# Performance work log

Measured on AMD Instinct MI355X. Metric: run time of the kernel, lower is better.

The kernel has to match this reference:

```python
import jax, jax.numpy as jnp
import numpy as np

EMBED = 2048
HEADS = 16
DFF = 4 * EMBED
EPS = 1e-5


def layernorm(x, g, b):
    mu = jnp.mean(x, axis=-1, keepdims=True)
    var = jnp.var(x, axis=-1, keepdims=True)
    return (x - mu) * jax.lax.rsqrt(var + EPS) * g + b


def setup_inputs() -> dict:
    key = jax.random.key(0)
    ks = jax.random.split(key, 16)
    s = 1.0 / np.sqrt(EMBED)
    sf = 1.0 / np.sqrt(DFF)
    return {
        "x": jax.random.normal(ks[0], (2, 2048, EMBED), jnp.float32),
        "Wq": jax.random.normal(ks[1], (EMBED, EMBED), jnp.float32) * s,
        "bq": jnp.zeros((EMBED,), jnp.float32),
        "Wk": jax.random.normal(ks[2], (EMBED, EMBED), jnp.float32) * s,
        "bk": jnp.zeros((EMBED,), jnp.float32),
        "Wv": jax.random.normal(ks[3], (EMBED, EMBED), jnp.float32) * s,
        "bv": jnp.zeros((EMBED,), jnp.float32),
        "Wo": jax.random.normal(ks[4], (EMBED, EMBED), jnp.float32) * s,
        "bo": jnp.zeros((EMBED,), jnp.float32),
        "g1": jnp.ones((EMBED,), jnp.float32),
        "b1": jnp.zeros((EMBED,), jnp.float32),
        "g2": jnp.ones((EMBED,), jnp.float32),
        "b2": jnp.zeros((EMBED,), jnp.float32),
        "W1": jax.random.normal(ks[5], (EMBED, DFF), jnp.float32) * s,
        "bf1": jnp.zeros((DFF,), jnp.float32),
        "W2": jax.random.normal(ks[6], (DFF, EMBED), jnp.float32) * sf,
        "bf2": jnp.zeros((EMBED,), jnp.float32),
    }


def reference(x, Wq, bq, Wk, bk, Wv, bv, Wo, bo, g1, b1, g2, b2, W1, bf1, W2, bf2):
    B, N, C = x.shape
    H = HEADS
    hd = C // H
    # QKV projections -> [B, H, N, hd]
    def split_heads(t):
        return t.reshape(B, N, H, hd).transpose(0, 2, 1, 3)
    q = split_heads(x @ Wq + bq)
    k = split_heads(x @ Wk + bk)
    v = split_heads(x @ Wv + bv)
    # scores [B, H, N, N]
    attn = jnp.einsum('bhqd,bhkd->bhqk', q, k) / np.sqrt(hd)
    attn = jax.nn.softmax(attn, axis=-1)
    out = jnp.einsum('bhqk,bhkd->bhqd', attn, v)
    out = out.transpose(0, 2, 1, 3).reshape(B, N, C)
    out = out @ Wo + bo
    h = layernorm(x + out, g1, b1)
    ff = jax.nn.gelu(h @ W1 + bf1, approximate=False) @ W2 + bf2
    return layernorm(h + ff, g2, b2)
```

## Files before the change

kernel.cpp:

```cpp
#include <hip/hip_runtime.h>
#include <math.h>

#define EMBED 2048
#define DFF   8192
#define TOK   4096
#define SEQ   2048
#define HEADS 16
#define HD    128
#define LDQ   6144

typedef __attribute__((ext_vector_type(8))) short short8;
typedef __attribute__((ext_vector_type(4))) float f32x4;

__device__ __forceinline__ unsigned short f2bf(float f) {
    unsigned int u = __float_as_uint(f);
    return (unsigned short)((u + 0x7FFFu + ((u >> 16) & 1u)) >> 16);
}
__device__ __forceinline__ float bf2f(unsigned short s) {
    return __uint_as_float(((unsigned int)s) << 16);
}
__device__ __forceinline__ float exp2_fast(float x) {
    return __builtin_amdgcn_exp2f(x);
}

__device__ __forceinline__ void async16(const void* g, void* l) {
    __builtin_amdgcn_global_load_lds((const __attribute__((address_space(1))) void*)g,
                                     (__attribute__((address_space(3))) void*)l, 16, 0, 0);
}

__device__ __forceinline__ float gelu_fast(float v) {
    const float y = 1.5957691216057308f * (v + 0.044715f * v * v * v);
    return v / (1.0f + __expf(-y));
}

template<int BM, int MODE>
__global__ __launch_bounds__(512, 2)
void gemm8p(const unsigned short* __restrict__ A, const unsigned short* __restrict__ B,
            const float* __restrict__ bias, const void* __restrict__ resid,
            unsigned short* __restrict__ C, int M, int N, int K, int lda)
{
    constexpr int ASLICE = BM * 32;
    constexpr int BSLICE = 256 * 32;
    constexpr int LA = BM / 128;
    constexpr int MF = BM / 32;
    __shared__ __align__(16) unsigned short sm[4*ASLICE + 4*BSLICE];

    const int t = threadIdx.x;
    const int w = t >> 6, l = t & 63;
    const int quad = l >> 4, m16 = l & 15;
    const int wm = w >> 2, wn = w & 3;

    const int nwg = gridDim.x * gridDim.y;
    const int orig = blockIdx.y * gridDim.x + blockIdx.x;
    const int lin = (orig & 7) * (nwg >> 3) + (orig >> 3);
    const int myt = lin % gridDim.y;
    const int nxt = lin / gridDim.y;
    const long bm = (long)myt * BM, bn = (long)nxt * 256;

    f32x4 acc[MF][4] = {};

    const unsigned short* Ag = A + (size_t)bm*lda;
    const unsigned short* Bg = B + (size_t)bn*K;

    auto stageA = [&](int buf, int ks, int k0) {
#pragma unroll
        for (int p = 0; p < LA; ++p) {
            const int e = p*512 + t;
            const int r = e >> 2, s = e & 3;
            const int gc = k0 + ks*32 + (s ^ ((r >> 1) & 3))*8;
            async16(Ag + (size_t)r*lda + gc,
                    sm + buf*2*ASLICE + ks*ASLICE + (p*512 + w*64)*8);
        }
    };
    auto stageB = [&](int buf, int ks, int k0) {
#pragma unroll
        for (int p = 0; p < 2; ++p) {
            const int e = p*512 + t;
            const int r = e >> 2, s = e & 3;
            const int gc = k0 + ks*32 + (s ^ ((r >> 1) & 3))*8;
            async16(Bg + (size_t)r*K + gc,
                    sm + 4*ASLICE + buf*2*BSLICE + ks*BSLICE + (p*512 + w*64)*8);
        }
    };

    stageA(0, 0, 0); stageB(0, 0, 0);
    stageA(0, 1, 0); stageB(0, 1, 0);

    const int iters = K >> 6;
    for (int it = 0; it < iters; ++it) {
        const int cur = it & 1;
        const bool pre = (it + 1 < iters);
        const int kn = (it + 1) << 6;

#pragma unroll
        for (int kk = 0; kk < 2; ++kk) {
            if (kk == 0 || pre) {
                if constexpr (BM == 256) asm volatile("s_waitcnt vmcnt(4)" ::: "memory");
                else                     asm volatile("s_waitcnt vmcnt(3)" ::: "memory");
            } else {
                asm volatile("s_waitcnt vmcnt(0)" ::: "memory");
            }
            __builtin_amdgcn_s_barrier();
            if (pre) { stageA(cur ^ 1, kk, kn); stageB(cur ^ 1, kk, kn); }

            const unsigned short* Ab = sm + cur*2*ASLICE + kk*ASLICE;
            const unsigned short* Bb = sm + 4*ASLICE + cur*2*BSLICE + kk*BSLICE;
            short8 afr[MF], bfr[4];
#pragma unroll
            for (int m = 0; m < MF; ++m) {
                const int R = wm*(BM/2) + m*16 + m16;
                const int sl = quad ^ ((R >> 1) & 3);
                afr[m] = *(const short8*)(Ab + R*32 + sl*8);
            }
#pragma unroll
            for (int n = 0; n < 4; ++n) {
                const int R = wn*64 + n*16 + m16;
                const int sl = quad ^ ((R >> 1) & 3);
                bfr[n] = *(const short8*)(Bb + R*32 + sl*8);
            }
            __builtin_amdgcn_s_setprio(1);
#pragma unroll
            for (int m = 0; m < MF; ++m)
#pragma unroll
                for (int n = 0; n < 4; ++n)
                    acc[m][n] = __builtin_amdgcn_mfma_f32_16x16x32_bf16(afr[m], bfr[n], acc[m][n], 0, 0, 0);
            __builtin_amdgcn_s_setprio(0);
        }
    }

    __syncthreads();
    asm volatile("" ::: "memory");
    float* Cs = (float*)sm;
    const int ecol = (t & 31) * 8;
    float bias8[8];
#pragma unroll
    for (int i = 0; i < 8; ++i) bias8[i] = bias[bn + ecol + i];

    constexpr int NP = BM / 64;
#pragma unroll
    for (int p = 0; p < NP; ++p) {
        if (p) __syncthreads();
        constexpr int HW = (NP == 4) ? 2 : 1;
        const int pwm = p / HW;
        const int mp = (NP == 4) ? (p & 1)*4 : 0;
        if (wm == pwm) {
#pragma unroll
            for (int mi = 0; mi < 4; ++mi)
#pragma unroll
                for (int n = 0; n < 4; ++n)
#pragma unroll
                    for (int r = 0; r < 4; ++r)
                        Cs[(mi*16 + quad*4 + r)*260 + wn*64 + n*16 + m16] = acc[mp + mi][n][r];
        }
        __syncthreads();
#pragma unroll
        for (int j = 0; j < 4; ++j) {
            const int row = j*16 + (t >> 5);
            float v[8];
            *(f32x4*)&v[0] = *(const f32x4*)&Cs[row*260 + ecol];
            *(f32x4*)&v[4] = *(const f32x4*)&Cs[row*260 + ecol + 4];
            const long gr = bm + p*64 + row;
            const long go = gr*N + bn + ecol;
            float r8[8];
            if (MODE == 1) {
                *(f32x4*)&r8[0] = *(const f32x4*)((const float*)resid + go);
                *(f32x4*)&r8[4] = *(const f32x4*)((const float*)resid + go + 4);
            }
            short8 rb16;
            if (MODE == 3) rb16 = *(const short8*)((const unsigned short*)resid + go);
            short8 o;
#pragma unroll
            for (int i = 0; i < 8; ++i) {
                float y = v[i] + bias8[i];
                if (MODE == 1) y += r8[i];
                if (MODE == 3) y += bf2f((unsigned short)rb16[i]);
                if (MODE == 2) y = gelu_fast(y);
                o[i] = (short)f2bf(y);
            }
            *(short8*)&C[go] = o;
        }
    }
}

__global__ __launch_bounds__(256, 2)
void attn_flash(unsigned short* __restrict__ qkv)
{
    __shared__ unsigned short Ks2[2][64*128];
    __shared__ unsigned short Vt2[2][128*72];
    __shared__ unsigned short Ps[4*16*72];

    const int t = threadIdx.x;
    const int w = t >> 6, l = t & 63;
    const int quad = l >> 4, m16 = l & 15;

    const int dd = blockIdx.x;
    const int bh = (dd & 7)*4 + ((dd >> 3) >> 4);
    const int qt = (dd >> 3) & 15;
    const int b = bh >> 4, h = bh & 15;

    const long rowq = (long)b*SEQ + qt*128;
    const long rowb = (long)b*SEQ;
    const int qc = h*HD;
    const int kc = EMBED + h*HD;
    const int vc = 2*EMBED + h*HD;

    const int rbase = w*4 + (l >> 4);
    const int slot  = l & 15;
    const int vslot = t & 15;
    const int vrp   = t >> 4;

    unsigned short* QsOv = (unsigned short*)Vt2;

    short8 va[2], vb[2];
#pragma unroll
    for (int u = 0; u < 2; ++u) {
        const int rp = u*16 + vrp;
        va[u] = *(const short8*)(qkv + (rowb + 2*rp    )*LDQ + vc + vslot*8);
        vb[u] = *(const short8*)(qkv + (rowb + 2*rp + 1)*LDQ + vc + vslot*8);
    }
#pragma unroll
    for (int u = 0; u < 8; ++u) {
        const int row = u*16 + rbase;
        const int c = slot ^ ((row >> 1) & 7);
        async16(qkv + (rowq + row)*LDQ + qc + c*8, QsOv + u*2048 + w*512);
    }
#pragma unroll
    for (int u = 0; u < 4; ++u) {
        const int row = u*16 + rbase;
        const int c = slot ^ ((row >> 1) & 7);
        async16(qkv + (rowb + row)*LDQ + kc + c*8, &Ks2[0][u*2048 + w*512]);
    }
    __syncthreads();

    short8 af[2][4];
#pragma unroll
    for (int qh = 0; qh < 2; ++qh)
#pragma unroll
        for (int ks = 0; ks < 4; ++ks) {
            const int row = w*32 + qh*16 + m16;
            const int sl = (4*ks + quad) ^ ((row >> 1) & 7);
            af[qh][ks] = *(const short8*)&QsOv[row*128 + sl*8];
        }
    __syncthreads();

#pragma unroll
    for (int u = 0; u < 2; ++u) {
        const int rp = u*16 + vrp;
#pragma unroll
        for (int i = 0; i < 8; ++i) {
            const int dv = vslot*8 + i;
            const int col = (2*rp) ^ (((dv >> 5) & 3) << 3);
            unsigned int pv = (unsigned int)(unsigned short)va[u][i] |
                              ((unsigned int)(unsigned short)vb[u][i] << 16);
            *(unsigned int*)&Vt2[0][dv*72 + col] = pv;
        }
    }
    __syncthreads();

    f32x4 O[2][8] = {};
    float mrun[2][4], lrun[2][4];
#pragma unroll
    for (int qh = 0; qh < 2; ++qh)
#pragma unroll
        for (int r = 0; r < 4; ++r) { mrun[qh][r] = -1e30f; lrun[qh][r] = 0.f; }
    unsigned short* Pw = Ps + w*16*72;
    const float SC = 0.08838834764831845f * 1.4426950408889634f;

    for (int kt = 0; kt < SEQ/64; ++kt) {
        const int cur = kt & 1;
        const bool pre = (kt + 1 < SEQ/64);
        const long rowkv = rowb + (long)(kt + 1)*64;

        if (pre) {
#pragma unroll
            for (int u = 0; u < 2; ++u) {
                const int rp = u*16 + vrp;
                va[u] = *(const short8*)(qkv + (rowkv + 2*rp    )*LDQ + vc + vslot*8);
                vb[u] = *(const short8*)(qkv + (rowkv + 2*rp + 1)*LDQ + vc + vslot*8);
            }
#pragma unroll
            for (int u = 0; u < 4; ++u) {
                const int row = u*16 + rbase;
                const int c = slot ^ ((row >> 1) & 7);
                async16(qkv + (rowkv + row)*LDQ + kc + c*8, &Ks2[cur^1][u*2048 + w*512]);
            }
        }

        f32x4 S[2][4];
#pragma unroll
        for (int ns = 0; ns < 4; ++ns) {
            f32x4 a0 = {0.f,0.f,0.f,0.f}, a1 = {0.f,0.f,0.f,0.f};
            const int row = ns*16 + m16;
            const int swr = (row >> 1) & 7;
#pragma unroll
            for (int ks = 0; ks < 4; ++ks) {
                const int sl = (4*ks + quad) ^ swr;
                const short8 bfr = *(const short8*)&Ks2[cur][row*128 + sl*8];
                a0 = __builtin_amdgcn_mfma_f32_16x16x32_bf16(af[0][ks], bfr, a0, 0, 0, 0);
                a1 = __builtin_amdgcn_mfma_f32_16x16x32_bf16(af[1][ks], bfr, a1, 0, 0, 0);
            }
#pragma unroll
            for (int r = 0; r < 4; ++r) { a0[r] *= SC; a1[r] *= SC; }
            S[0][ns] = a0; S[1][ns] = a1;
        }

#pragma unroll
        for (int qh = 0; qh < 2; ++qh) {
            float al[4], rs4[4];
#pragma unroll
            for (int r = 0; r < 4; ++r) {
                float tm = fmaxf(fmaxf(S[qh][0][r], S[qh][1][r]), fmaxf(S[qh][2][r], S[qh][3][r]));
                tm = fmaxf(tm, __shfl_xor(tm, 1));
                tm = fmaxf(tm, __shfl_xor(tm, 2));
                tm = fmaxf(tm, __shfl_xor(tm, 4));
                tm = fmaxf(tm, __shfl_xor(tm, 8));
                const float mn = fmaxf(mrun[qh][r], tm);
                al[r] = exp2_fast(mrun[qh][r] - mn);
                mrun[qh][r] = mn;
                rs4[r] = 0.f;
            }
#pragma unroll
            for (int ns = 0; ns < 4; ++ns)
#pragma unroll
                for (int r = 0; r < 4; ++r) {
                    const float p = exp2_fast(S[qh][ns][r] - mrun[qh][r]);
                    rs4[r] += p;
                    Pw[(quad*4 + r)*72 + ns*16 + m16] = f2bf(p);
                }
#pragma unroll
            for (int r = 0; r < 4; ++r) {
                rs4[r] += __shfl_xor(rs4[r], 1);
                rs4[r] += __shfl_xor(rs4[r], 2);
                rs4[r] += __shfl_xor(rs4[r], 4);
                rs4[r] += __shfl_xor(rs4[r], 8);
                lrun[qh][r] = lrun[qh][r]*al[r] + rs4[r];
            }
            if (__any((al[0] != 1.f) | (al[1] != 1.f) | (al[2] != 1.f) | (al[3] != 1.f))) {
#pragma unroll
                for (int i = 0; i < 8; ++i)
#pragma unroll
                    for (int r = 0; r < 4; ++r) O[qh][i][r] *= al[r];
            }

            if (qh == 1 && pre) {
#pragma unroll
                for (int u = 0; u < 2; ++u) {
                    const int rp = u*16 + vrp;
#pragma unroll
                    for (int i = 0; i < 8; ++i) {
                        const int dv = vslot*8 + i;
                        const int col = (2*rp) ^ (((dv >> 5) & 3) << 3);
                        unsigned int pv = (unsigned int)(unsigned short)va[u][i] |
                                          ((unsigned int)(unsigned short)vb[u][i] << 16);
                        *(unsigned int*)&Vt2[cur^1][dv*72 + col] = pv;
                    }
                }
            }

#pragma unroll
            for (int ks2 = 0; ks2 < 2; ++ks2) {
                const short8 ap = *(const short8*)&Pw[m16*72 + ks2*32 + quad*8];
#pragma unroll
                for (int ds = 0; ds < 8; ++ds) {
                    const int dv = ds*16 + m16;
                    const int jcol = (ks2*32 + quad*8) ^ (((dv >> 5) & 3) << 3);
                    const short8 bv = *(const short8*)&Vt2[cur][dv*72 + jcol];
                    O[qh][ds] = __builtin_amdgcn_mfma_f32_16x16x32_bf16(ap, bv, O[qh][ds], 0, 0, 0);
                }
            }
        }

        __syncthreads();
    }

    float inv[2][4];
#pragma unroll
    for (int qh = 0; qh < 2; ++qh)
#pragma unroll
        for (int r = 0; r < 4; ++r) inv[qh][r] = 1.0f / lrun[qh][r];
#pragma unroll
    for (int qh = 0; qh < 2; ++qh)
#pragma unroll
        for (int ds = 0; ds < 8; ++ds)
#pragma unroll
            for (int r = 0; r < 4; ++r) {
                const long row = rowq + w*32 + qh*16 + quad*4 + r;
                qkv[row*LDQ + qc + ds*16 + m16] = f2bf(O[qh][ds][r] * inv[qh][r]);
            }
}

template<int OUTF32>
__global__ __launch_bounds__(256)
void ln_bf16(const unsigned short* __restrict__ X, const float* __restrict__ g,
             const float* __restrict__ be, void* __restrict__ Y)
{
    __shared__ float r1[256], r2[256];
    const int t = threadIdx.x;
    const long row = blockIdx.x;
    const unsigned short* x = X + row*EMBED;
    float v[8];
    const short8 xv = *(const short8*)(x + t*8);
    float s = 0.f, s2 = 0.f;
#pragma unroll
    for (int i = 0; i < 8; ++i) {
        v[i] = bf2f((unsigned short)xv[i]);
        s += v[i]; s2 += v[i]*v[i];
    }
    r1[t] = s; r2[t] = s2;
    __syncthreads();
    for (int k = 128; k > 0; k >>= 1) {
        if (t < k) { r1[t] += r1[t+k]; r2[t] += r2[t+k]; }
        __syncthreads();
    }
    const float mu = r1[0] * (1.0f/EMBED);
    const float var = r2[0] * (1.0f/EMBED) - mu*mu;
    const float rstd = rsqrtf(var + 1e-5f);
    if (OUTF32) {
        float* y = (float*)Y + row*EMBED + t*8;
#pragma unroll
        for (int i = 0; i < 8; ++i) y[i] = (v[i]-mu)*rstd*g[t*8+i] + be[t*8+i];
    } else {
        unsigned short* y = (unsigned short*)Y + row*EMBED;
        short8 o;
#pragma unroll
        for (int i = 0; i < 8; ++i) o[i] = (short)f2bf((v[i]-mu)*rstd*g[t*8+i] + be[t*8+i]);
        *(short8*)(y + t*8) = o;
    }
}

__global__ __launch_bounds__(256)
void cvt_transpose(const float* __restrict__ W, unsigned short* __restrict__ Wt, int K, int N)
{
    __shared__ unsigned short T[32][33];
    const int t = threadIdx.x;
    const long n0 = (long)blockIdx.x*32, k0 = (long)blockIdx.y*32;
    {
        const int r = t >> 3, c = (t & 7)*4;
        const float4 vv = *(const float4*)&W[(k0 + r)*N + n0 + c];
        T[r][c+0] = f2bf(vv.x); T[r][c+1] = f2bf(vv.y);
        T[r][c+2] = f2bf(vv.z); T[r][c+3] = f2bf(vv.w);
    }
    __syncthreads();
    const int rn = t >> 3, kk = (t & 7)*4;
    unsigned int p0 = (unsigned int)T[kk+0][rn] | ((unsigned int)T[kk+1][rn] << 16);
    unsigned int p1 = (unsigned int)T[kk+2][rn] | ((unsigned int)T[kk+3][rn] << 16);
    unsigned int* dst = (unsigned int*)&Wt[(n0 + rn)*K + k0 + kk];
    dst[0] = p0; dst[1] = p1;
}

__global__ __launch_bounds__(256)
void cvt_f32_bf16(const float* __restrict__ X, unsigned short* __restrict__ Y, long n)
{
    const long i = ((long)blockIdx.x*256 + threadIdx.x)*8;
    if (i >= n) return;
    const float4 a = *(const float4*)&X[i];
    const float4 b = *(const float4*)&X[i+4];
    short8 o;
    o[0]=(short)f2bf(a.x); o[1]=(short)f2bf(a.y); o[2]=(short)f2bf(a.z); o[3]=(short)f2bf(a.w);
    o[4]=(short)f2bf(b.x); o[5]=(short)f2bf(b.y); o[6]=(short)f2bf(b.z); o[7]=(short)f2bf(b.w);
    *(short8*)&Y[i] = o;
}

__global__ __launch_bounds__(256)
void concat_bias(const float* __restrict__ bq, const float* __restrict__ bk,
                 const float* __restrict__ bv, float* __restrict__ out)
{
    const int i = blockIdx.x*256 + threadIdx.x;
    if (i < 2048) out[i] = bq[i];
    else if (i < 4096) out[i] = bk[i-2048];
    else if (i < 6144) out[i] = bv[i-4096];
}

extern "C" void kernel_launch(void* const* d_in, const int* in_sizes, int n_in,
                              void* d_out, int out_size, void* d_ws, size_t ws_size,
                              hipStream_t stream)
{
    const float* x   = (const float*)d_in[0];
    const float* Wq  = (const float*)d_in[1];
    const float* bq  = (const float*)d_in[2];
    const float* Wk  = (const float*)d_in[3];
    const float* bk  = (const float*)d_in[4];
    const float* Wv  = (const float*)d_in[5];
    const float* bv  = (const float*)d_in[6];
    const float* Wo  = (const float*)d_in[7];
    const float* bo  = (const float*)d_in[8];
    const float* g1  = (const float*)d_in[9];
    const float* b1  = (const float*)d_in[10];
    const float* g2v = (const float*)d_in[11];
    const float* b2v = (const float*)d_in[12];
    const float* W1  = (const float*)d_in[13];
    const float* bf1 = (const float*)d_in[14];
    const float* W2  = (const float*)d_in[15];
    const float* bf2 = (const float*)d_in[16];
    float* out = (float*)d_out;

    char* ws = (char*)d_ws;
    unsigned short* Wqkvt = (unsigned short*)(ws + 0);
    unsigned short* Wot   = (unsigned short*)(ws + 25165824);
    unsigned short* W1t   = (unsigned short*)(ws + 33554432);
    unsigned short* W2t   = (unsigned short*)(ws + 67108864);
    float*          bqkv  = (float*)         (ws + 100663296);
    char* arenaA = ws + 100687872;
    unsigned short* xb   = (unsigned short*)(arenaA);
    unsigned short* qkv  = (unsigned short*)(arenaA + 16777216);
    unsigned short* res1 = (unsigned short*)(arenaA);
    unsigned short* ff   = (unsigned short*)(arenaA);
    unsigned short* hb   = (unsigned short*)(ws + 167796736);
    unsigned short* res2 = (unsigned short*)(ws + 0);

    const dim3 blk(256);
    const dim3 blk8(512);

    cvt_transpose<<<dim3(64,64),  blk, 0, stream>>>(Wq, Wqkvt,             2048, 2048);
    cvt_transpose<<<dim3(64,64),  blk, 0, stream>>>(Wk, Wqkvt + 2048*2048, 2048, 2048);
    cvt_transpose<<<dim3(64,64),  blk, 0, stream>>>(Wv, Wqkvt + 2*2048*2048, 2048, 2048);
    cvt_transpose<<<dim3(64,64),  blk, 0, stream>>>(Wo, Wot, 2048, 2048);
    cvt_transpose<<<dim3(256,64), blk, 0, stream>>>(W1, W1t, 2048, 8192);
    cvt_transpose<<<dim3(64,256), blk, 0, stream>>>(W2, W2t, 8192, 2048);
    concat_bias<<<dim3(24), blk, 0, stream>>>(bq, bk, bv, bqkv);
    cvt_f32_bf16<<<dim3(4096), blk, 0, stream>>>(x, xb, (long)TOK*EMBED);

    gemm8p<128,0><<<dim3(24,32), blk8, 0, stream>>>(xb, Wqkvt, bqkv, nullptr, qkv, TOK, 6144, 2048, 2048);
    attn_flash<<<dim3(512), blk, 0, stream>>>(qkv);
    gemm8p<128,1><<<dim3(8,32), blk8, 0, stream>>>(qkv, Wot, bo, x, res1, TOK, 2048, 2048, 6144);
    ln_bf16<0><<<dim3(4096), blk, 0, stream>>>(res1, g1, b1, hb);
    gemm8p<256,2><<<dim3(32,16), blk8, 0, stream>>>(hb, W1t, bf1, nullptr, ff, TOK, 8192, 2048, 2048);
    gemm8p<128,3><<<dim3(8,32), blk8, 0, stream>>>(ff, W2t, bf2, hb, res2, TOK, 2048, 8192, 8192);
    ln_bf16<1><<<dim3(4096), blk, 0, stream>>>(res2, g2v, b2v, out);
}
```

Before: 912.2 us.

## Single-buffer V tile and share V fragments across both query halves

Merges shared arrays into one buffer with a single V tile, and stores P for both query halves so each V fragment read from LDS feeds two MFMAs. The next V tile is written after an added barrier instead of being double-buffered. This halves V LDS reads and cuts LDS footprint, at the cost of an extra barrier per iteration and less overlap of the V store with compute.

After: 917.2 us. No clear change (+0.5%).

```diff
diff --git a/kernel.cpp b/kernel.cpp
--- a/kernel.cpp
+++ b/kernel.cpp
@@ -185,9 +185,11 @@
 __global__ __launch_bounds__(256, 2)
 void attn_flash(unsigned short* __restrict__ qkv)
 {
-    __shared__ unsigned short Ks2[2][64*128];
-    __shared__ unsigned short Vt2[2][128*72];
-    __shared__ unsigned short Ps[4*16*72];
+    __shared__ __align__(16) unsigned short smem[34816];
+    unsigned short* Ks2  = smem;
+    unsigned short* Vt   = smem + 16384;
+    unsigned short* Ps   = smem + 25600;
+    unsigned short* QsOv = smem + 16384;
 
     const int t = threadIdx.x;
     const int w = t >> 6, l = t & 63;
@@ -209,8 +211,6 @@
     const int vslot = t & 15;
     const int vrp   = t >> 4;
 
-    unsigned short* QsOv = (unsigned short*)Vt2;
-
     short8 va[2], vb[2];
 #pragma unroll
     for (int u = 0; u < 2; ++u) {
@@ -228,7 +228,7 @@
     for (int u = 0; u < 4; ++u) {
         const int row = u*16 + rbase;
         const int c = slot ^ ((row >> 1) & 7);
-        async16(qkv + (rowb + row)*LDQ + kc + c*8, &Ks2[0][u*2048 + w*512]);
+        async16(qkv + (rowb + row)*LDQ + kc + c*8, Ks2 + u*2048 + w*512);
     }
     __syncthreads();
 
@@ -252,7 +252,7 @@
             const int col = (2*rp) ^ (((dv >> 5) & 3) << 3);
             unsigned int pv = (unsigned int)(unsigned short)va[u][i] |
                               ((unsigned int)(unsigned short)vb[u][i] << 16);
-            *(unsigned int*)&Vt2[0][dv*72 + col] = pv;
+            *(unsigned int*)&Vt[dv*72 + col] = pv;
         }
     }
     __syncthreads();
@@ -263,7 +263,7 @@
     for (int qh = 0; qh < 2; ++qh)
 #pragma unroll
         for (int r = 0; r < 4; ++r) { mrun[qh][r] = -1e30f; lrun[qh][r] = 0.f; }
-    unsigned short* Pw = Ps + w*16*72;
+    unsigned short* Pw = Ps + w*2304;
     const float SC = 0.08838834764831845f * 1.4426950408889634f;
 
     for (int kt = 0; kt < SEQ/64; ++kt) {
@@ -282,7 +282,8 @@
             for (int u = 0; u < 4; ++u) {
                 const int row = u*16 + rbase;
                 const int c = slot ^ ((row >> 1) & 7);
-                async16(qkv + (rowkv + row)*LDQ + kc + c*8, &Ks2[cur^1][u*2048 + w*512]);
+                async16(qkv + (rowkv + row)*LDQ + kc + c*8,
+                        Ks2 + (cur^1)*8192 + u*2048 + w*512);
             }
         }
 
@@ -295,7 +296,7 @@
 #pragma unroll
             for (int ks = 0; ks < 4; ++ks) {
                 const int sl = (4*ks + quad) ^ swr;
-                const short8 bfr = *(const short8*)&Ks2[cur][row*128 + sl*8];
+                const short8 bfr = *(const short8*)&Ks2[cur*8192 + row*128 + sl*8];
                 a0 = __builtin_amdgcn_mfma_f32_16x16x32_bf16(af[0][ks], bfr, a0, 0, 0, 0);
                 a1 = __builtin_amdgcn_mfma_f32_16x16x32_bf16(af[1][ks], bfr, a1, 0, 0, 0);
             }
@@ -325,7 +326,7 @@
                 for (int r = 0; r < 4; ++r) {
                     const float p = exp2_fast(S[qh][ns][r] - mrun[qh][r]);
                     rs4[r] += p;
-                    Pw[(quad*4 + r)*72 + ns*16 + m16] = f2bf(p);
+                    Pw[(qh*16 + quad*4 + r)*72 + ns*16 + m16] = f2bf(p);
                 }
 #pragma unroll
             for (int r = 0; r < 4; ++r) {
@@ -341,35 +342,37 @@
 #pragma unroll
                     for (int r = 0; r < 4; ++r) O[qh][i][r] *= al[r];
             }
-
-            if (qh == 1 && pre) {
-#pragma unroll
-                for (int u = 0; u < 2; ++u) {
-                    const int rp = u*16 + vrp;
-#pragma unroll
-                    for (int i = 0; i < 8; ++i) {
-                        const int dv = vslot*8 + i;
-                        const int col = (2*rp) ^ (((dv >> 5) & 3) << 3);
-                        unsigned int pv = (unsigned int)(unsigned short)va[u][i] |
-                                          ((unsigned int)(unsigned short)vb[u][i] << 16);
-                        *(unsigned int*)&Vt2[cur^1][dv*72 + col] = pv;
-                    }
+        }
+
+#pragma unroll
+        for (int ks2 = 0; ks2 < 2; ++ks2) {
+            const short8 ap0 = *(const short8*)&Pw[(m16     )*72 + ks2*32 + quad*8];
+            const short8 ap1 = *(const short8*)&Pw[(16 + m16)*72 + ks2*32 + quad*8];
+#pragma unroll
+            for (int ds = 0; ds < 8; ++ds) {
+                const int dv = ds*16 + m16;
+                const int jcol = (ks2*32 + quad*8) ^ (((dv >> 5) & 3) << 3);
+                const short8 bv = *(const short8*)&Vt[dv*72 + jcol];
+                O[0][ds] = __builtin_amdgcn_mfma_f32_16x16x32_bf16(ap0, bv, O[0][ds], 0, 0, 0);
+                O[1][ds] = __builtin_amdgcn_mfma_f32_16x16x32_bf16(ap1, bv, O[1][ds], 0, 0, 0);
+            }
+        }
+
+        __syncthreads();
+        if (pre) {
+#pragma unroll
+            for (int u = 0; u < 2; ++u) {
+                const int rp = u*16 + vrp;
+#pragma unroll
+                for (int i = 0; i < 8; ++i) {
+                    const int dv = vslot*8 + i;
+                    const int col = (2*rp) ^ (((dv >> 5) & 3) << 3);
+                    unsigned int pv = (unsigned int)(unsigned short)va[u][i] |
+                                      ((unsigned int)(unsigned short)vb[u][i] << 16);
+                    *(unsigned int*)&Vt[dv*72 + col] = pv;
                 }
             }
-
-#pragma unroll
-            for (int ks2 = 0; ks2 < 2; ++ks2) {
-                const short8 ap = *(const short8*)&Pw[m16*72 + ks2*32 + quad*8];
-#pragma unroll
-                for (int ds = 0; ds < 8; ++ds) {
-                    const int dv = ds*16 + m16;
-                    const int jcol = (ks2*32 + quad*8) ^ (((dv >> 5) & 3) << 3);
-                    const short8 bv = *(const short8*)&Vt2[cur][dv*72 + jcol];
-                    O[qh][ds] = __builtin_amdgcn_mfma_f32_16x16x32_bf16(ap, bv, O[qh][ds], 0, 0, 0);
-                }
-            }
-        }
-
+        }
         __syncthreads();
     }
 
```
